# Kernel optimization log

Measured on AMD Instinct MI355X. Metric: run time of the kernel, lower is better.

Reference implementation:

```python
import jax, jax.numpy as jnp
import numpy as np

HIDDEN_DIM = 128
ATTN_DIM = 64
B, N = 2, 512

def setup_inputs() -> dict:
    key = jax.random.key(0)
    ks = jax.random.split(key, 8)
    s = 0.05
    return {
        "X":    jax.random.normal(ks[0], (B, N, HIDDEN_DIM), dtype=jnp.float32),
        "Wo":   jax.random.normal(ks[1], (ATTN_DIM, HIDDEN_DIM), dtype=jnp.float32) * s,
        "W1":   jax.random.normal(ks[2], (ATTN_DIM, HIDDEN_DIM), dtype=jnp.float32) * s,
        "Wphi": jax.random.normal(ks[3], (ATTN_DIM,), dtype=jnp.float32) * s,
        "Wy":   jax.random.normal(ks[4], (HIDDEN_DIM, HIDDEN_DIM), dtype=jnp.float32) * s,
        "by":   jax.random.normal(ks[5], (HIDDEN_DIM,), dtype=jnp.float32) * s,
        "We":   jax.random.normal(ks[6], (HIDDEN_DIM, ATTN_DIM), dtype=jnp.float32) * s,
        "be":   jax.random.normal(ks[7], (HIDDEN_DIM,), dtype=jnp.float32) * s,
    }

def reference(X, Wo, W1, Wphi, Wy, by, We, be):
    # h_o, h_1: [B, N, A]
    h_o = jnp.einsum('bnc,ac->bna', X, Wo)
    h_1 = jnp.einsum('bnc,ac->bna', X, W1)
    # pairwise tanh edge features e_ij: [B, N, N, A]
    e = jnp.tanh(h_o[:, :, None, :] + h_1[:, None, :, :])
    # scores [B, N, N] via w_phi projection, row-wise softmax over j
    scores = jnp.einsum('bija,a->bij', e, Wphi)
    alpha = jax.nn.softmax(scores, axis=-1)
    # value path 1: Wy x_j -> aggregated by alpha (bmm)
    X_y = jnp.einsum('bnc,hc->bnh', X, Wy) + by
    part1 = jnp.einsum('bij,bjh->bih', alpha, X_y)
    # value path 2: We e_ij -> weighted sum over j
    eval_ = jnp.einsum('bija,ha->bijh', e, We) + be  # [B, N, N, H]
    part2 = jnp.einsum('bij,bijh->bih', alpha, eval_)
    return part1 + part2
```

## Files before the change

### kernel.cpp

```cpp
#include <hip/hip_runtime.h>

#define B_ 2
#define N_ 512
#define C_ 128
#define A_ 64
#define H_ 128

#define SC2L 2.885390081777927f
#define NEG2LE -2.885390081777927f

#define OFF_WOT 0
#define OFF_W1T (OFF_WOT + C_*A_)
#define OFF_WYT (OFF_W1T + C_*A_)
#define OFF_WET (OFF_WYT + C_*H_)
#define OFF_V   (OFF_WET + A_*H_)
#define OFF_UT8 (OFF_V   + B_*N_*A_)
#define OFF_US8 (OFF_UT8 + B_*N_*A_/2)
#define OFF_XYP (OFF_US8 + B_*N_*A_/2)

__device__ __forceinline__ float fexp2(float x) { return __builtin_amdgcn_exp2f(x); }
__device__ __forceinline__ float frcp(float x)  { return __builtin_amdgcn_rcpf(x); }
__device__ __forceinline__ unsigned f2bf(float x) {
  unsigned u = __float_as_uint(x);
  return (u + 0x7fffu + ((u >> 16) & 1u)) >> 16;
}
__device__ __forceinline__ float bf_lo(unsigned d) { return __uint_as_float(d << 16); }
__device__ __forceinline__ float bf_hi(unsigned d) { return __uint_as_float(d & 0xffff0000u); }

__global__ __launch_bounds__(256) void prep_weights(
    const float* __restrict__ Wo, const float* __restrict__ W1,
    const float* __restrict__ Wy, const float* __restrict__ We,
    float* __restrict__ ws) {
  int t = blockIdx.x * 256 + threadIdx.x;
  if (t < A_*C_) {
    int a = t / C_, c = t % C_;
    ws[OFF_WOT + c*A_ + a] = Wo[t];
    ws[OFF_W1T + c*A_ + a] = W1[t];
    int h2 = t / A_, a2 = t % A_;
    ws[OFF_WET + a2*H_ + h2] = We[t];
  }
  if (t < H_*C_) {
    int h = t / C_, c = t % C_;
    ws[OFF_WYT + c*H_ + h] = Wy[t];
  }
}

__global__ __launch_bounds__(256) void proj_kernel(
    const float* __restrict__ X, const float* __restrict__ by,
    float* __restrict__ ws) {
  __shared__ float xs[2*C_];
  int row0 = blockIdx.x * 2;
  int t = threadIdx.x;
  if (t < 2*C_) xs[t] = X[(size_t)row0*C_ + t];
  __syncthreads();

  const float* wt;
  int col, stride;
  if (t < 64)       { wt = ws + OFF_WOT; col = t;       stride = A_; }
  else if (t < 128) { wt = ws + OFF_W1T; col = t - 64;  stride = A_; }
  else              { wt = ws + OFF_WYT; col = t - 128; stride = H_; }

  float acc0 = 0.f, acc1 = 0.f;
  #pragma unroll 8
  for (int c = 0; c < C_; ++c) {
    float wv = wt[c*stride + col];
    acc0 = fmaf(xs[c], wv, acc0);
    acc1 = fmaf(xs[C_ + c], wv, acc1);
  }

  int b = row0 >> 9, n0 = row0 & (N_-1);

  if (t < 64) {
    float* o = ws + OFF_V + (size_t)row0*A_ + col;
    o[0] = fexp2(SC2L * acc0);
    o[A_] = fexp2(SC2L * acc1);
  } else if (t < 128) {
    int a = col;
    unsigned u0 = f2bf(fexp2(SC2L * acc0));
    unsigned u1 = f2bf(fexp2(SC2L * acc1));
    unsigned short* ut = (unsigned short*)(ws + OFF_UT8);
    size_t bA = ((size_t)(b*8 + (a >> 3))*N_ + n0)*8 + (a & 7);
    ut[bA] = (unsigned short)u0;
    ut[bA + 8] = (unsigned short)u1;
    unsigned short* us = (unsigned short*)(ws + OFF_US8);
    size_t bC = ((size_t)(b*64 + (n0 >> 3))*A_ + a)*8 + (n0 & 7);
    us[bC] = (unsigned short)u0;
    us[bC + 1] = (unsigned short)u1;
  } else {
    int h = col;
    float bb = by[h];
    unsigned x0 = f2bf(acc0 + bb);
    unsigned x1 = f2bf(acc1 + bb);
    unsigned* xp = (unsigned*)(ws + OFF_XYP);
    xp[(size_t)(b*(N_/2) + (n0 >> 1))*H_ + h] = x0 | (x1 << 16);
  }
}

__global__ __launch_bounds__(512) void attn_kernel(
    const float* __restrict__ Wphi, const float* __restrict__ be,
    const float* __restrict__ ws, float* __restrict__ out) {
  __shared__ __align__(16) float pkv[A_];
  __shared__ __align__(16) float pkw[A_];
  __shared__ float sc[N_];
  __shared__ float reds[8];
  __shared__ float ebw[8][A_];
  __shared__ float ebar[A_];
  __shared__ __align__(16) float p1s[16][H_];

  int t = threadIdx.x;
  int w = t >> 6, lane = t & 63;
  int bi = blockIdx.x;
  int b = bi >> 9, i = bi & (N_-1);

  const uint4* ut8 = (const uint4*)((const unsigned short*)(ws + OFF_UT8))
                     + (size_t)b*8*N_;
  const uint4* us8 = (const uint4*)((const unsigned short*)(ws + OFF_US8))
                     + (size_t)b*64*A_;
  const uint4* xy4 = (const uint4*)((const unsigned*)(ws + OFF_XYP))
                     + (size_t)b*(N_/2)*(H_/4);
  const float* wet = ws + OFF_WET;

  if (t < A_) {
    pkv[t] = ws[OFF_V + (size_t)(b*N_ + i)*A_ + t];
    pkw[t] = Wphi[t];
  }
  __syncthreads();

  float s = 0.f;
  {
    const float4* pv4 = (const float4*)pkv;
    const float4* pw4 = (const float4*)pkw;
    #pragma unroll
    for (int g = 0; g < 8; ++g) {
      uint4 d = ut8[(size_t)g*N_ + t];
      float4 v0 = pv4[2*g], v1 = pv4[2*g + 1];
      float4 w0 = pw4[2*g], w1 = pw4[2*g + 1];
      s = fmaf(w0.x, frcp(fmaf(v0.x, bf_lo(d.x), 1.f)), s);
      s = fmaf(w0.y, frcp(fmaf(v0.y, bf_hi(d.x), 1.f)), s);
      s = fmaf(w0.z, frcp(fmaf(v0.z, bf_lo(d.y), 1.f)), s);
      s = fmaf(w0.w, frcp(fmaf(v0.w, bf_hi(d.y), 1.f)), s);
      s = fmaf(w1.x, frcp(fmaf(v1.x, bf_lo(d.z), 1.f)), s);
      s = fmaf(w1.y, frcp(fmaf(v1.y, bf_hi(d.z), 1.f)), s);
      s = fmaf(w1.z, frcp(fmaf(v1.z, bf_lo(d.w), 1.f)), s);
      s = fmaf(w1.w, frcp(fmaf(v1.w, bf_hi(d.w), 1.f)), s);
    }
  }
  float p = fexp2(NEG2LE * s);
  sc[t] = p;
  float q = p;
  #pragma unroll
  for (int m = 1; m < 64; m <<= 1) q += __shfl_xor(q, m);
  if (lane == 0) reds[w] = q;
  __syncthreads();

  {
    float v = pkv[lane];
    const float4* sc4 = (const float4*)sc;
    float c = 0.f;
    #pragma unroll
    for (int oo = 0; oo < 8; ++oo) {
      int o = oo*8 + w;
      uint4 d = us8[(size_t)o*A_ + lane];
      float4 pA = sc4[o*2], pB = sc4[o*2 + 1];
      c = fmaf(pA.x, frcp(fmaf(v, bf_lo(d.x), 1.f)), c);
      c = fmaf(pA.y, frcp(fmaf(v, bf_hi(d.x), 1.f)), c);
      c = fmaf(pA.z, frcp(fmaf(v, bf_lo(d.y), 1.f)), c);
      c = fmaf(pA.w, frcp(fmaf(v, bf_hi(d.y), 1.f)), c);
      c = fmaf(pB.x, frcp(fmaf(v, bf_lo(d.z), 1.f)), c);
      c = fmaf(pB.y, frcp(fmaf(v, bf_hi(d.z), 1.f)), c);
      c = fmaf(pB.z, frcp(fmaf(v, bf_lo(d.w), 1.f)), c);
      c = fmaf(pB.w, frcp(fmaf(v, bf_hi(d.w), 1.f)), c);
    }
    ebw[w][lane] = c;
  }

  {
    int h4 = t & 31, qd = t >> 5;
    float d0 = 0.f, d1 = 0.f, d2 = 0.f, d3 = 0.f;
    #pragma unroll
    for (int kc = 0; kc < 16; ++kc) {
      int k = qd*16 + kc;
      uint4 d = xy4[(size_t)k*(H_/4) + h4];
      float pa = sc[2*k], pb = sc[2*k + 1];
      d0 = fmaf(pa, bf_lo(d.x), d0); d0 = fmaf(pb, bf_hi(d.x), d0);
      d1 = fmaf(pa, bf_lo(d.y), d1); d1 = fmaf(pb, bf_hi(d.y), d1);
      d2 = fmaf(pa, bf_lo(d.z), d2); d2 = fmaf(pb, bf_hi(d.z), d2);
      d3 = fmaf(pa, bf_lo(d.w), d3); d3 = fmaf(pb, bf_hi(d.w), d3);
    }
    *(float4*)&p1s[qd][h4*4] = make_float4(d0, d1, d2, d3);
  }
  __syncthreads();

  if (t < A_) {
    float e = 0.f;
    #pragma unroll
    for (int k = 0; k < 8; ++k) e += ebw[k][t];
    float l = 0.f;
    #pragma unroll
    for (int k = 0; k < 8; ++k) l += reds[k];
    ebar[t] = l - 2.0f*e;
  }
  __syncthreads();

  if (t < H_) {
    int h = t;
    float l = 0.f;
    #pragma unroll
    for (int k = 0; k < 8; ++k) l += reds[k];
    float acc = 0.f;
    #pragma unroll
    for (int k = 0; k < 16; ++k) acc += p1s[k][h];
    float e2 = 0.f;
    #pragma unroll 8
    for (int a = 0; a < A_; ++a) e2 = fmaf(ebar[a], wet[a*H_ + h], e2);
    out[(size_t)bi*H_ + h] = (acc + e2) * frcp(l) + be[h];
  }
}

extern "C" void kernel_launch(void* const* d_in, const int* in_sizes, int n_in,
                              void* d_out, int out_size, void* d_ws, size_t ws_size,
                              hipStream_t stream) {
  const float* X    = (const float*)d_in[0];
  const float* Wo   = (const float*)d_in[1];
  const float* W1   = (const float*)d_in[2];
  const float* Wphi = (const float*)d_in[3];
  const float* Wy   = (const float*)d_in[4];
  const float* by   = (const float*)d_in[5];
  const float* We   = (const float*)d_in[6];
  const float* be   = (const float*)d_in[7];
  float* out = (float*)d_out;
  float* ws  = (float*)d_ws;

  hipLaunchKernelGGL(prep_weights, dim3(64), dim3(256), 0, stream, Wo, W1, Wy, We, ws);
  hipLaunchKernelGGL(proj_kernel, dim3(B_*N_/2), dim3(256), 0, stream, X, by, ws);
  hipLaunchKernelGGL(attn_kernel, dim3(B_*N_), dim3(512), 0, stream, Wphi, be, ws, out);
}
```

Baseline: 92.48 us.

## Process two query rows per attention block to reuse loaded key/value data

The attention kernel now handles two query rows per block with 1024 threads, halving the grid. In the e-bar and part1 phases, each loaded bf16 key column and X_y tile is applied to both rows, so global/L2 traffic per output row is halved. In exchange each block is larger, uses more shared memory and registers, and has fewer blocks to spread across CUs, which can lower occupancy.

```diff
diff --git a/kernel.cpp b/kernel.cpp
--- a/kernel.cpp
+++ b/kernel.cpp
@@ -89,28 +89,30 @@
   } else {
     int h = col;
     float bb = by[h];
-    unsigned x0 = f2bf(acc0 + bb);
-    unsigned x1 = f2bf(acc1 + bb);
+    unsigned xv0 = f2bf(acc0 + bb);
+    unsigned xv1 = f2bf(acc1 + bb);
     unsigned* xp = (unsigned*)(ws + OFF_XYP);
-    xp[(size_t)(b*(N_/2) + (n0 >> 1))*H_ + h] = x0 | (x1 << 16);
-  }
-}
-
-__global__ __launch_bounds__(512) void attn_kernel(
+    xp[(size_t)(b*(N_/2) + (n0 >> 1))*H_ + h] = xv0 | (xv1 << 16);
+  }
+}
+
+__global__ __launch_bounds__(1024) void attn_kernel(
     const float* __restrict__ Wphi, const float* __restrict__ be,
     const float* __restrict__ ws, float* __restrict__ out) {
-  __shared__ __align__(16) float pkv[A_];
+  __shared__ __align__(16) float pkv[2][A_];
   __shared__ __align__(16) float pkw[A_];
-  __shared__ float sc[N_];
-  __shared__ float reds[8];
-  __shared__ float ebw[8][A_];
-  __shared__ float ebar[A_];
-  __shared__ __align__(16) float p1s[16][H_];
+  __shared__ float sc[2][N_];
+  __shared__ float reds[16];
+  __shared__ float ebw[2][16][A_];
+  __shared__ float ebar[2][A_];
+  __shared__ __align__(16) float p1s[2][32][H_];
 
   int t = threadIdx.x;
   int w = t >> 6, lane = t & 63;
-  int bi = blockIdx.x;
-  int b = bi >> 9, i = bi & (N_-1);
+  int blk = blockIdx.x;
+  int b = blk >> 8;
+  int i0 = (blk & 255) * 2;
+  int g0 = b*N_ + i0;
 
   const uint4* ut8 = (const uint4*)((const unsigned short*)(ws + OFF_UT8))
                      + (size_t)b*8*N_;
@@ -120,19 +122,22 @@
                      + (size_t)b*(N_/2)*(H_/4);
   const float* wet = ws + OFF_WET;
 
-  if (t < A_) {
-    pkv[t] = ws[OFF_V + (size_t)(b*N_ + i)*A_ + t];
-    pkw[t] = Wphi[t];
-  }
-  __syncthreads();
-
-  float s = 0.f;
+  if (t < 2*A_) {
+    int r = t >> 6, a = t & 63;
+    pkv[r][a] = ws[OFF_V + (size_t)(g0 + r)*A_ + a];
+  } else if (t < 3*A_) {
+    pkw[t - 2*A_] = Wphi[t - 2*A_];
+  }
+  __syncthreads();
+
   {
-    const float4* pv4 = (const float4*)pkv;
+    int r = t >> 9, j = t & 511;
+    const float4* pv4 = (const float4*)pkv[r];
     const float4* pw4 = (const float4*)pkw;
+    float s = 0.f;
     #pragma unroll
     for (int g = 0; g < 8; ++g) {
-      uint4 d = ut8[(size_t)g*N_ + t];
+      uint4 d = ut8[(size_t)g*N_ + j];
       float4 v0 = pv4[2*g], v1 = pv4[2*g + 1];
       float4 w0 = pw4[2*g], w1 = pw4[2*g + 1];
       s = fmaf(w0.x, frcp(fmaf(v0.x, bf_lo(d.x), 1.f)), s);
@@ -144,76 +149,103 @@
       s = fmaf(w1.z, frcp(fmaf(v1.z, bf_lo(d.w), 1.f)), s);
       s = fmaf(w1.w, frcp(fmaf(v1.w, bf_hi(d.w), 1.f)), s);
     }
-  }
-  float p = fexp2(NEG2LE * s);
-  sc[t] = p;
-  float q = p;
-  #pragma unroll
-  for (int m = 1; m < 64; m <<= 1) q += __shfl_xor(q, m);
-  if (lane == 0) reds[w] = q;
+    float p = fexp2(NEG2LE * s);
+    sc[r][j] = p;
+    float q = p;
+    #pragma unroll
+    for (int m = 1; m < 64; m <<= 1) q += __shfl_xor(q, m);
+    if (lane == 0) reds[w] = q;
+  }
   __syncthreads();
 
   {
-    float v = pkv[lane];
-    const float4* sc4 = (const float4*)sc;
-    float c = 0.f;
-    #pragma unroll
-    for (int oo = 0; oo < 8; ++oo) {
-      int o = oo*8 + w;
+    float v0 = pkv[0][lane], v1 = pkv[1][lane];
+    const float4* s40 = (const float4*)sc[0];
+    const float4* s41 = (const float4*)sc[1];
+    float c0 = 0.f, c1 = 0.f;
+    #pragma unroll
+    for (int oo = 0; oo < 4; ++oo) {
+      int o = oo*16 + w;
       uint4 d = us8[(size_t)o*A_ + lane];
-      float4 pA = sc4[o*2], pB = sc4[o*2 + 1];
-      c = fmaf(pA.x, frcp(fmaf(v, bf_lo(d.x), 1.f)), c);
-      c = fmaf(pA.y, frcp(fmaf(v, bf_hi(d.x), 1.f)), c);
-      c = fmaf(pA.z, frcp(fmaf(v, bf_lo(d.y), 1.f)), c);
-      c = fmaf(pA.w, frcp(fmaf(v, bf_hi(d.y), 1.f)), c);
-      c = fmaf(pB.x, frcp(fmaf(v, bf_lo(d.z), 1.f)), c);
-      c = fmaf(pB.y, frcp(fmaf(v, bf_hi(d.z), 1.f)), c);
-      c = fmaf(pB.z, frcp(fmaf(v, bf_lo(d.w), 1.f)), c);
-      c = fmaf(pB.w, frcp(fmaf(v, bf_hi(d.w), 1.f)), c);
+      float u0 = bf_lo(d.x), u1 = bf_hi(d.x), u2 = bf_lo(d.y), u3 = bf_hi(d.y);
+      float u4 = bf_lo(d.z), u5 = bf_hi(d.z), u6 = bf_lo(d.w), u7 = bf_hi(d.w);
+      float4 pA0 = s40[o*2], pB0 = s40[o*2 + 1];
+      float4 pA1 = s41[o*2], pB1 = s41[o*2 + 1];
+      float r0 = frcp(fmaf(v0, u0, 1.f)), q0 = frcp(fmaf(v1, u0, 1.f));
+      float r1 = frcp(fmaf(v0, u1, 1.f)), q1 = frcp(fmaf(v1, u1, 1.f));
+      float r2 = frcp(fmaf(v0, u2, 1.f)), q2 = frcp(fmaf(v1, u2, 1.f));
+      float r3 = frcp(fmaf(v0, u3, 1.f)), q3 = frcp(fmaf(v1, u3, 1.f));
+      float r4 = frcp(fmaf(v0, u4, 1.f)), q4 = frcp(fmaf(v1, u4, 1.f));
+      float r5 = frcp(fmaf(v0, u5, 1.f)), q5 = frcp(fmaf(v1, u5, 1.f));
+      float r6 = frcp(fmaf(v0, u6, 1.f)), q6 = frcp(fmaf(v1, u6, 1.f));
+      float r7 = frcp(fmaf(v0, u7, 1.f)), q7 = frcp(fmaf(v1, u7, 1.f));
+      c0 = fmaf(pA0.x, r0, c0); c1 = fmaf(pA1.x, q0, c1);
+      c0 = fmaf(pA0.y, r1, c0); c1 = fmaf(pA1.y, q1, c1);
+      c0 = fmaf(pA0.z, r2, c0); c1 = fmaf(pA1.z, q2, c1);
+      c0 = fmaf(pA0.w, r3, c0); c1 = fmaf(pA1.w, q3, c1);
+      c0 = fmaf(pB0.x, r4, c0); c1 = fmaf(pB1.x, q4, c1);
+      c0 = fmaf(pB0.y, r5, c0); c1 = fmaf(pB1.y, q5, c1);
+      c0 = fmaf(pB0.z, r6, c0); c1 = fmaf(pB1.z, q6, c1);
+      c0 = fmaf(pB0.w, r7, c0); c1 = fmaf(pB1.w, q7, c1);
     }
-    ebw[w][lane] = c;
+    ebw[0][w][lane] = c0;
+    ebw[1][w][lane] = c1;
   }
 
   {
     int h4 = t & 31, qd = t >> 5;
     float d0 = 0.f, d1 = 0.f, d2 = 0.f, d3 = 0.f;
-    #pragma unroll
-    for (int kc = 0; kc < 16; ++kc) {
-      int k = qd*16 + kc;
+    float e0 = 0.f, e1 = 0.f, e2 = 0.f, e3 = 0.f;
+    const float2* p20 = (const float2*)sc[0];
+    const float2* p21 = (const float2*)sc[1];
+    #pragma unroll
+    for (int kc = 0; kc < 8; ++kc) {
+      int k = qd*8 + kc;
       uint4 d = xy4[(size_t)k*(H_/4) + h4];
-      float pa = sc[2*k], pb = sc[2*k + 1];
-      d0 = fmaf(pa, bf_lo(d.x), d0); d0 = fmaf(pb, bf_hi(d.x), d0);
-      d1 = fmaf(pa, bf_lo(d.y), d1); d1 = fmaf(pb, bf_hi(d.y), d1);
-      d2 = fmaf(pa, bf_lo(d.z), d2); d2 = fmaf(pb, bf_hi(d.z), d2);
-      d3 = fmaf(pa, bf_lo(d.w), d3); d3 = fmaf(pb, bf_hi(d.w), d3);
+      float2 P0 = p20[k];
+      float2 P1 = p21[k];
+      float xa = bf_lo(d.x), xb = bf_hi(d.x);
+      float xc = bf_lo(d.y), xd = bf_hi(d.y);
+      float xe = bf_lo(d.z), xf = bf_hi(d.z);
+      float xg = bf_lo(d.w), xh = bf_hi(d.w);
+      d0 = fmaf(P0.x, xa, d0); d0 = fmaf(P0.y, xb, d0);
+      d1 = fmaf(P0.x, xc, d1); d1 = fmaf(P0.y, xd, d1);
+      d2 = fmaf(P0.x, xe, d2); d2 = fmaf(P0.y, xf, d2);
+      d3 = fmaf(P0.x, xg, d3); d3 = fmaf(P0.y, xh, d3);
+      e0 = fmaf(P1.x, xa, e0); e0 = fmaf(P1.y, xb, e0);
+      e1 = fmaf(P1.x, xc, e1); e1 = fmaf(P1.y, xd, e1);
+      e2 = fmaf(P1.x, xe, e2); e2 = fmaf(P1.y, xf, e2);
+      e3 = fmaf(P1.x, xg, e3); e3 = fmaf(P1.y, xh, e3);
     }
-    *(float4*)&p1s[qd][h4*4] = make_float4(d0, d1, d2, d3);
-  }
-  __syncthreads();
-
-  if (t < A_) {
+    *(float4*)&p1s[0][qd][h4*4] = make_float4(d0, d1, d2, d3);
+    *(float4*)&p1s[1][qd][h4*4] = make_float4(e0, e1, e2, e3);
+  }
+  __syncthreads();
+
+  if (t < 2*A_) {
+    int r = t >> 6, a = t & 63;
     float e = 0.f;
     #pragma unroll
-    for (int k = 0; k < 8; ++k) e += ebw[k][t];
+    for (int k = 0; k < 16; ++k) e += ebw[r][k][a];
     float l = 0.f;
     #pragma unroll
-    for (int k = 0; k < 8; ++k) l += reds[k];
-    ebar[t] = l - 2.0f*e;
-  }
-  __syncthreads();
-
-  if (t < H_) {
-    int h = t;
+    for (int k = 0; k < 8; ++k) l += reds[r*8 + k];
+    ebar[r][a] = l - 2.0f*e;
+  }
+  __syncthreads();
+
+  if (t < 2*H_) {
+    int r = t >> 7, h = t & 127;
     float l = 0.f;
     #pragma unroll
-    for (int k = 0; k < 8; ++k) l += reds[k];
+    for (int k = 0; k < 8; ++k) l += reds[r*8 + k];
     float acc = 0.f;
     #pragma unroll
-    for (int k = 0; k < 16; ++k) acc += p1s[k][h];
+    for (int k = 0; k < 32; ++k) acc += p1s[r][k][h];
     float e2 = 0.f;
     #pragma unroll 8
-    for (int a = 0; a < A_; ++a) e2 = fmaf(ebar[a], wet[a*H_ + h], e2);
-    out[(size_t)bi*H_ + h] = (acc + e2) * frcp(l) + be[h];
+    for (int a = 0; a < A_; ++a) e2 = fmaf(ebar[r][a], wet[a*H_ + h], e2);
+    out[(size_t)(g0 + r)*H_ + h] = (acc + e2) * frcp(l) + be[h];
   }
 }
 
@@ -233,5 +265,5 @@
 
   hipLaunchKernelGGL(prep_weights, dim3(64), dim3(256), 0, stream, Wo, W1, Wy, We, ws);
   hipLaunchKernelGGL(proj_kernel, dim3(B_*N_/2), dim3(256), 0, stream, X, by, ws);
-  hipLaunchKernelGGL(attn_kernel, dim3(B_*N_), dim3(512), 0, stream, Wphi, be, ws, out);
-}
+  hipLaunchKernelGGL(attn_kernel, dim3(B_*N_/2), dim3(1024), 0, stream, Wphi, be, ws, out);
+}
```

New measurement: 92.77 us (median of 2 runs). About the same (+0.3%).
